# Kernel tuning notes

Measured on AMD Instinct MI355X. Metric: run time of the kernel, lower is better.

## Reference

```python
import jax, jax.numpy as jnp
import numpy as np

B, T, C, HS = 8, 2048, 768, 256  # batch, seq(block_size), n_embed, head_size


def setup_inputs() -> dict:
    key = jax.random.key(0)
    kx, kq, kk, kv = jax.random.split(key, 4)
    scale = 1.0 / np.sqrt(C)
    return {
        "x": jax.random.normal(kx, (B, T, C), dtype=jnp.float32),
        # torch nn.Linear(n_embed, head_size, bias=False) computes x @ W.T;
        # store weights pre-transposed as [in, out].
        "Wq": jax.random.normal(kq, (C, HS), dtype=jnp.float32) * scale,
        "Wk": jax.random.normal(kk, (C, HS), dtype=jnp.float32) * scale,
        "Wv": jax.random.normal(kv, (C, HS), dtype=jnp.float32) * scale,
    }


def reference(x, Wq, Wk, Wv):
    Bx, Tx, Cx = x.shape
    q = x @ Wq  # [B,T,HS]
    k = x @ Wk  # [B,T,HS]
    v = x @ Wv  # [B,T,HS]
    # NOTE: original scales by C**-0.5 with C = n_embed (not head_size)
    att = jnp.einsum('btd,bsd->bts', q, k) * (Cx ** -0.5)  # [B,T,T]
    causal = jnp.tril(jnp.ones((Tx, Tx), dtype=bool))
    att = jnp.where(causal, att, -jnp.inf)
    probs = jax.nn.softmax(att, axis=-1)
    # dropout=0.0 -> identity (eval mode)
    out = jnp.einsum('bts,bsd->btd', probs, v)  # [B,T,HS]
    return out
```

## Files before the change

kernel.cpp:

```cpp
#include <hip/hip_runtime.h>
#include <hip/hip_bf16.h>
#include <math.h>

#define B_  8
#define T_  2048
#define C_  768
#define HS_ 256

#define CHUNKS_PER_BATCH 72
#define NSLOT (CHUNKS_PER_BATCH * B_)

typedef float  f32x4  __attribute__((ext_vector_type(4)));
typedef __bf16 bf16x8 __attribute__((ext_vector_type(8)));
typedef __bf16 bf16x4 __attribute__((ext_vector_type(4)));
typedef __bf16 bf16x2 __attribute__((ext_vector_type(2)));

#define MFMA16(a, b, c) __builtin_amdgcn_mfma_f32_16x16x32_bf16((a), (b), (c), 0, 0, 0)

#define GLOAD_LDS16(gp, lp)                                                     \
    __builtin_amdgcn_global_load_lds(                                           \
        (const __attribute__((address_space(1))) void*)(gp),                    \
        (__attribute__((address_space(3))) void*)(lp), 16, 0, 0)

__device__ __forceinline__ int chunk_cum128(int qb) {
    int g = qb >> 1;
    return g * (g + 1) + (qb & 1) * (g + 1);
}

__global__ __launch_bounds__(256) void prep_kernel(const float* __restrict__ x,
                                                   const float* __restrict__ Wq,
                                                   const float* __restrict__ Wk,
                                                   const float* __restrict__ Wv,
                                                   __bf16* __restrict__ xb,
                                                   __bf16* __restrict__ wt_all,
                                                   float qscale) {
    const int bid = blockIdx.x;
    if (bid < 6144) {
        size_t i = ((size_t)bid * 256 + threadIdx.x) * 8;
        f32x4 a = *(const f32x4*)(x + i);
        f32x4 b = *(const f32x4*)(x + i + 4);
        bf16x8 o;
        o[0] = (__bf16)a[0]; o[1] = (__bf16)a[1]; o[2] = (__bf16)a[2]; o[3] = (__bf16)a[3];
        o[4] = (__bf16)b[0]; o[5] = (__bf16)b[1]; o[6] = (__bf16)b[2]; o[7] = (__bf16)b[3];
        *(bf16x8*)(xb + i) = o;
    } else {
        int idx = (bid - 6144) * 256 + threadIdx.x;
        int n   = idx & 255;
        int t   = idx >> 8;
        int mat = t / 96;
        int k8  = t - mat * 96;
        const float* W = (mat == 0) ? Wq : ((mat == 1) ? Wk : Wv);
        float scale = (mat == 0) ? qscale : 1.0f;
        bf16x8 o;
#pragma unroll
        for (int j = 0; j < 8; j++)
            o[j] = (__bf16)(W[(k8 * 8 + j) * HS_ + n] * scale);
        *(bf16x8*)&wt_all[((size_t)mat * HS_ + n) * C_ + k8 * 8] = o;
    }
}

__global__ __launch_bounds__(256) void proj_kernel(const __bf16* __restrict__ xb,
                                                   const __bf16* __restrict__ wt,
                                                   __bf16* __restrict__ qf_,
                                                   __bf16* __restrict__ kf_,
                                                   __bf16* __restrict__ vf_) {
    __shared__ alignas(16) __bf16 ldsA[2][128 * 32];
    __shared__ alignas(16) __bf16 ldsB[2][128 * 32];

    const int tid  = threadIdx.x;
    const int w    = tid >> 6;
    const int lane = tid & 63;
    const int cm   = lane & 15;
    const int quad = lane >> 4;
    const int wm   = w & 1;
    const int wn   = w >> 1;
    const int m0   = blockIdx.x * 128;
    const int n0   = blockIdx.y * 128;
    const int mat  = n0 >> 8;

    f32x4 acc[4][4];
#pragma unroll
    for (int i = 0; i < 4; i++)
#pragma unroll
        for (int j = 0; j < 4; j++) acc[i][j] = (f32x4){0.f, 0.f, 0.f, 0.f};

#pragma unroll
    for (int h = 0; h < 2; h++) {
        int c = tid + h * 256;
        GLOAD_LDS16(xb + (size_t)(m0 + (c >> 2)) * C_ + (c & 3) * 8, &ldsA[0][c * 8]);
        GLOAD_LDS16(wt + (size_t)(n0 + (c >> 2)) * C_ + (c & 3) * 8, &ldsB[0][c * 8]);
    }

    for (int kt = 0; kt < 24; kt++) {
        const int cur = kt & 1;
        __syncthreads();

        if (kt < 23) {
            const int k0 = (kt + 1) * 32;
#pragma unroll
            for (int h = 0; h < 2; h++) {
                int c = tid + h * 256;
                GLOAD_LDS16(xb + (size_t)(m0 + (c >> 2)) * C_ + k0 + (c & 3) * 8,
                            &ldsA[cur ^ 1][c * 8]);
                GLOAD_LDS16(wt + (size_t)(n0 + (c >> 2)) * C_ + k0 + (c & 3) * 8,
                            &ldsB[cur ^ 1][c * 8]);
            }
        }

        bf16x8 af[4], bfr[4];
#pragma unroll
        for (int mt = 0; mt < 4; mt++)
            af[mt] = *(const bf16x8*)&ldsA[cur][(wm * 64 + mt * 16 + cm) * 32 + quad * 8];
#pragma unroll
        for (int nt = 0; nt < 4; nt++)
            bfr[nt] = *(const bf16x8*)&ldsB[cur][(wn * 64 + nt * 16 + cm) * 32 + quad * 8];
        if (mat < 2) {
#pragma unroll
            for (int dt = 0; dt < 4; dt++)
#pragma unroll
                for (int qt2 = 0; qt2 < 4; qt2++)
                    acc[dt][qt2] = MFMA16(bfr[dt], af[qt2], acc[dt][qt2]);
        } else {
#pragma unroll
            for (int mt = 0; mt < 4; mt++)
#pragma unroll
                for (int nt = 0; nt < 4; nt++)
                    acc[mt][nt] = MFMA16(af[mt], bfr[nt], acc[mt][nt]);
        }
    }

    const int dBase = (n0 & 255) + wn * 64;
    const int b     = m0 >> 11;
    if (mat < 2) {
        const int rt2 = ((m0 & 2047) >> 6) + wm;
        __bf16* dst = (mat == 0) ? qf_ : kf_;
#pragma unroll
        for (int dt = 0; dt < 4; dt++)
#pragma unroll
            for (int qt2 = 0; qt2 < 4; qt2++) {
                int d0    = dBase + dt * 16 + quad * 4;
                int ksq   = d0 >> 5;
                int quadp = (d0 >> 3) & 3;
                int j0    = d0 & 7;
                size_t addr;
                if (mat == 0)
                    addr = ((((size_t)(b * 32 + rt2) * 4 + qt2) * 8 + ksq) * 64
                            + quadp * 16 + cm) * 8 + j0;
                else
                    addr = ((((size_t)(b * 32 + rt2) * 8 + ksq) * 4 + qt2) * 64
                            + quadp * 16 + cm) * 8 + j0;
                bf16x4 v4;
                v4[0] = (__bf16)acc[dt][qt2][0]; v4[1] = (__bf16)acc[dt][qt2][1];
                v4[2] = (__bf16)acc[dt][qt2][2]; v4[3] = (__bf16)acc[dt][qt2][3];
                *(bf16x4*)(dst + addr) = v4;
            }
    } else {
        const int rt = ((m0 & 2047) + wm * 64) >> 6;
#pragma unroll
        for (int mt = 0; mt < 4; mt++) {
            int ks2   = (mt >> 1) & 1;
            int quadF = (mt & 1) * 2 + (quad >> 1);
            int jb    = (quad & 1) * 4;
#pragma unroll
            for (int nt = 0; nt < 4; nt++) {
                int ntv = (dBase >> 4) + nt;
                size_t idx = ((((size_t)(b * 32 + rt) * 2 + ks2) * 16 + ntv) * 64
                              + quadF * 16 + cm) * 8 + jb;
                bf16x4 v4;
                v4[0] = (__bf16)acc[mt][nt][0]; v4[1] = (__bf16)acc[mt][nt][1];
                v4[2] = (__bf16)acc[mt][nt][2]; v4[3] = (__bf16)acc[mt][nt][3];
                *(bf16x4*)(vf_ + idx) = v4;
            }
        }
    }
}

__global__ __launch_bounds__(256, 2) void flash_part(const __bf16* __restrict__ qf_,
                                                     const __bf16* __restrict__ kf_,
                                                     const __bf16* __restrict__ vf_,
                                                     __bf16* __restrict__ Opart,
                                                     float* __restrict__ mpart,
                                                     float* __restrict__ lpart) {
    __shared__ alignas(16) __bf16 ldsK[2][8 * 2 * 64 * 8];
    __shared__ alignas(16) __bf16 ldsV[2][16 * 64 * 8];
    __shared__ alignas(16) __bf16 ldsP[4][2][512];

    const int tid  = threadIdx.x;
    const int w    = tid >> 6;
    const int lane = tid & 63;
    const int cm   = lane & 15;
    const int quad = lane >> 4;

    const int pid  = blockIdx.x;
    const int b    = pid & 7;
    const int r    = (CHUNKS_PER_BATCH - 1) - (pid >> 3);
    int qb = 0, ci = 0;
    {
        int rr = r;
        for (int j = 0; j < 16; j++) {
            int c = (j >> 1) + 1;
            if (rr < c) { qb = j; ci = rr; break; }
            rr -= c;
        }
    }
    const int lpid = b * CHUNKS_PER_BATCH + r;
    const int kt_begin = ci * 8;
    const int kt_end   = min(kt_begin + 8, 4 * qb + 4);

    bf16x8 qf2[2][8];
#pragma unroll
    for (int qg = 0; qg < 2; qg++) {
        int g16 = qb * 8 + w * 2 + qg;
        const __bf16* qp = qf_ + (((size_t)(b * 32 + (g16 >> 2)) * 4 + (g16 & 3)) * 8) * 512
                           + lane * 8;
#pragma unroll
        for (int ks = 0; ks < 8; ks++) qf2[qg][ks] = *(const bf16x8*)(qp + ks * 512);
    }

    auto stage = [&](int bsel, int kt) {
        const int kt64 = kt >> 1, kh = kt & 1;
        const __bf16* kgb = kf_ + (((size_t)(b * 32 + kt64) * 8) * 4 + kh * 2) * 512;
#pragma unroll
        for (int h = 0; h < 4; h++) {
            int g = h * 256 + tid;
            int ks = g >> 7, sub = g & 127;
            GLOAD_LDS16(kgb + (size_t)ks * 4 * 512 + sub * 8,
                        &ldsK[bsel][(h * 256 + w * 64) * 8]);
        }
        const __bf16* vgb = vf_ + ((size_t)(b * 64 + kt) * 16) * 512;
#pragma unroll
        for (int h = 0; h < 4; h++) {
            int g = h * 256 + tid;
            GLOAD_LDS16(vgb + (size_t)g * 8,
                        &ldsV[bsel][(h * 256 + w * 64) * 8]);
        }
    };

    f32x4 accO[2][16];
#pragma unroll
    for (int qg = 0; qg < 2; qg++)
#pragma unroll
        for (int i = 0; i < 16; i++) accO[qg][i] = (f32x4){0.f, 0.f, 0.f, 0.f};
    float mi[2] = {0.f, 0.f}, li[2] = {0.f, 0.f};

    const int wrow = qb * 128 + w * 32;

    stage(0, kt_begin);
    asm volatile("s_waitcnt vmcnt(0)" ::: "memory");
    __builtin_amdgcn_s_barrier();

    int cur = 0;
    for (int kt = kt_begin; kt < kt_end; kt++) {
        if (kt + 1 < kt_end) stage(cur ^ 1, kt + 1);

        f32x4 s[2][2];
#pragma unroll
        for (int ns = 0; ns < 2; ns++)
#pragma unroll
            for (int qg = 0; qg < 2; qg++) s[ns][qg] = (f32x4){0.f, 0.f, 0.f, 0.f};
        __builtin_amdgcn_s_setprio(1);
#pragma unroll
        for (int ns = 0; ns < 2; ns++)
#pragma unroll
            for (int ks = 0; ks < 8; ks++) {
                bf16x8 kfr = *(const bf16x8*)&ldsK[cur][(ks * 2 + ns) * 512 + lane * 8];
                s[ns][0] = MFMA16(kfr, qf2[0][ks], s[ns][0]);
                s[ns][1] = MFMA16(kfr, qf2[1][ks], s[ns][1]);
            }
        __builtin_amdgcn_s_setprio(0);
        if (kt * 32 + 31 > wrow) {
#pragma unroll
            for (int qg = 0; qg < 2; qg++) {
                int qglob = wrow + qg * 16 + cm;
#pragma unroll
                for (int ns = 0; ns < 2; ns++)
#pragma unroll
                    for (int i = 0; i < 4; i++)
                        if (kt * 32 + ns * 16 + quad * 4 + i > qglob)
                            s[ns][qg][i] = -__builtin_inff();
            }
        }
        if (kt == kt_begin) {
#pragma unroll
            for (int qg = 0; qg < 2; qg++) {
                float pm = -__builtin_inff();
#pragma unroll
                for (int ns = 0; ns < 2; ns++)
#pragma unroll
                    for (int i = 0; i < 4; i++) pm = fmaxf(pm, s[ns][qg][i]);
                pm = fmaxf(pm, __shfl_xor(pm, 16));
                pm = fmaxf(pm, __shfl_xor(pm, 32));
                mi[qg] = pm;
            }
        }
        float p[2][2][4];
        float rs[2] = {0.f, 0.f};
#pragma unroll
        for (int qg = 0; qg < 2; qg++)
#pragma unroll
            for (int ns = 0; ns < 2; ns++)
#pragma unroll
                for (int i = 0; i < 4; i++) {
                    p[qg][ns][i] = exp2f(s[ns][qg][i] - mi[qg]);
                    rs[qg] += p[qg][ns][i];
                }
#pragma unroll
        for (int qg = 0; qg < 2; qg++) {
            rs[qg] += __shfl_xor(rs[qg], 16);
            rs[qg] += __shfl_xor(rs[qg], 32);
            li[qg] += rs[qg];
        }

#pragma unroll
        for (int qg = 0; qg < 2; qg++)
#pragma unroll
            for (int ns = 0; ns < 2; ns++)
#pragma unroll
                for (int i2 = 0; i2 < 2; i2++) {
                    bf16x2 d2;
                    d2[0] = (__bf16)p[qg][ns][2 * i2];
                    d2[1] = (__bf16)p[qg][ns][2 * i2 + 1];
                    int off = ((ns * 2 + (quad >> 1)) * 16 + cm) * 8
                              + (quad & 1) * 4 + i2 * 2;
                    *(bf16x2*)&ldsP[w][qg][off] = d2;
                }
        bf16x8 pf0 = *(const bf16x8*)&ldsP[w][0][(quad * 16 + cm) * 8];
        bf16x8 pf1 = *(const bf16x8*)&ldsP[w][1][(quad * 16 + cm) * 8];
        __builtin_amdgcn_s_setprio(1);
#pragma unroll
        for (int nt = 0; nt < 16; nt++) {
            bf16x8 vfr = *(const bf16x8*)&ldsV[cur][(nt * 64 + lane) * 8];
            accO[0][nt] = MFMA16(vfr, pf0, accO[0][nt]);
            accO[1][nt] = MFMA16(vfr, pf1, accO[1][nt]);
        }
        __builtin_amdgcn_s_setprio(0);

        asm volatile("s_waitcnt vmcnt(0)" ::: "memory");
        __builtin_amdgcn_s_barrier();
        cur ^= 1;
    }

#pragma unroll
    for (int qg = 0; qg < 2; qg++) {
        __bf16* op = Opart + ((size_t)lpid * 128 + w * 32 + qg * 16 + cm) * HS_;
#pragma unroll
        for (int nt = 0; nt < 16; nt++) {
            bf16x4 v4;
            v4[0] = (__bf16)accO[qg][nt][0]; v4[1] = (__bf16)accO[qg][nt][1];
            v4[2] = (__bf16)accO[qg][nt][2]; v4[3] = (__bf16)accO[qg][nt][3];
            *(bf16x4*)(op + nt * 16 + quad * 4) = v4;
        }
        if (quad == 0) {
            mpart[lpid * 128 + w * 32 + qg * 16 + cm] = mi[qg];
            lpart[lpid * 128 + w * 32 + qg * 16 + cm] = li[qg];
        }
    }
}

__global__ __launch_bounds__(256) void flash_combine(const __bf16* __restrict__ Opart,
                                                     const float* __restrict__ mpart,
                                                     const float* __restrict__ lpart,
                                                     float* __restrict__ out) {
    const int b    = blockIdx.x >> 4;
    const int qb   = blockIdx.x & 15;
    const int nc   = (qb >> 1) + 1;
    const int pid0 = b * CHUNKS_PER_BATCH + chunk_cum128(qb);

    const int tid  = threadIdx.x;
    const int col  = (tid & 63) * 4;
    const int r0   = blockIdx.y * 16 + (tid >> 6) * 4;

    f32x4 ms = (f32x4){-__builtin_inff(), -__builtin_inff(),
                       -__builtin_inff(), -__builtin_inff()};
    for (int c = 0; c < nc; c++) {
        f32x4 m4 = *(const f32x4*)(mpart + (pid0 + c) * 128 + r0);
#pragma unroll
        for (int i = 0; i < 4; i++) ms[i] = fmaxf(ms[i], m4[i]);
    }
    f32x4 acc[4];
#pragma unroll
    for (int i = 0; i < 4; i++) acc[i] = (f32x4){0.f, 0.f, 0.f, 0.f};
    f32x4 lt = (f32x4){0.f, 0.f, 0.f, 0.f};
    for (int c = 0; c < nc; c++) {
        f32x4 m4 = *(const f32x4*)(mpart + (pid0 + c) * 128 + r0);
        f32x4 l4 = *(const f32x4*)(lpart + (pid0 + c) * 128 + r0);
#pragma unroll
        for (int i = 0; i < 4; i++) {
            float sc = exp2f(m4[i] - ms[i]);
            lt[i] += l4[i] * sc;
            bf16x4 o = *(const bf16x4*)(Opart
                        + ((size_t)(pid0 + c) * 128 + r0 + i) * HS_ + col);
            acc[i][0] += (float)o[0] * sc; acc[i][1] += (float)o[1] * sc;
            acc[i][2] += (float)o[2] * sc; acc[i][3] += (float)o[3] * sc;
        }
    }
#pragma unroll
    for (int i = 0; i < 4; i++) {
        float inv = 1.0f / lt[i];
        f32x4 res = (f32x4){acc[i][0] * inv, acc[i][1] * inv,
                            acc[i][2] * inv, acc[i][3] * inv};
        *(f32x4*)(out + ((size_t)(b * T_ + qb * 128 + r0 + i)) * HS_ + col) = res;
    }
}

extern "C" void kernel_launch(void* const* d_in, const int* in_sizes, int n_in,
                              void* d_out, int out_size, void* d_ws, size_t ws_size,
                              hipStream_t stream) {
    const float* x  = (const float*)d_in[0];
    const float* Wq = (const float*)d_in[1];
    const float* Wk = (const float*)d_in[2];
    const float* Wv = (const float*)d_in[3];
    float* out = (float*)d_out;

    char* ws = (char*)d_ws;
    size_t off = 0;
    __bf16* wt_all = (__bf16*)(ws + off); off += 1179648;
    __bf16* qfrag  = (__bf16*)(ws + off); off += 8388608;
    __bf16* kfrag  = (__bf16*)(ws + off); off += 8388608;
    __bf16* vfrag  = (__bf16*)(ws + off); off += 8388608;
    __bf16* xb     = (__bf16*)(ws + off);
    __bf16* Opart  = (__bf16*)(ws + off); off += (size_t)NSLOT * 128 * HS_ * 2;
    float*  mpart  = (float*)(ws + off);  off += (size_t)NSLOT * 128 * 4;
    float*  lpart  = (float*)(ws + off);

    float qscale = 1.4426950408889634f / sqrtf((float)C_);

    prep_kernel<<<dim3(6432), 256, 0, stream>>>(x, Wq, Wk, Wv, xb, wt_all, qscale);
    proj_kernel<<<dim3(128, 6), 256, 0, stream>>>(xb, wt_all, qfrag, kfrag, vfrag);
    flash_part<<<dim3(NSLOT), 256, 0, stream>>>(qfrag, kfrag, vfrag, Opart, mpart, lpart);
    flash_combine<<<dim3(128, 8), 256, 0, stream>>>(Opart, mpart, lpart, out);
}
```

Measured before the change: 187.6 us.

## Decouple waves in flash_part with per-wave 32-row chunks and private LDS

Each wave now owns its own 32-query-row work item with its own key range and its own LDS slot, instead of four waves sharing a 128-row block with a double-buffered K/V tile and block-wide barriers. K and V are loaded into a single per-wave buffer one after the other, so each wave waits on its own loads but never on a barrier. This removes barrier stalls and the extra work of waves whose rows are already past the causal diagonal. In exchange, K/V tiles are no longer shared across the four waves, so global/L2 traffic rises, and load latency is only partly hidden. The combine kernel is rewritten to merge the finer 32-row partials.

```diff
diff --git a/kernel.cpp b/kernel.cpp
--- a/kernel.cpp
+++ b/kernel.cpp
@@ -7,8 +7,8 @@
 #define C_  768
 #define HS_ 256
 
-#define CHUNKS_PER_BATCH 72
-#define NSLOT (CHUNKS_PER_BATCH * B_)
+#define WAVES_PER_BATCH 288
+#define NSLOT (WAVES_PER_BATCH * B_)
 
 typedef float  f32x4  __attribute__((ext_vector_type(4)));
 typedef __bf16 bf16x8 __attribute__((ext_vector_type(8)));
@@ -21,11 +21,6 @@
     __builtin_amdgcn_global_load_lds(                                           \
         (const __attribute__((address_space(1))) void*)(gp),                    \
         (__attribute__((address_space(3))) void*)(lp), 16, 0, 0)
-
-__device__ __forceinline__ int chunk_cum128(int qb) {
-    int g = qb >> 1;
-    return g * (g + 1) + (qb & 1) * (g + 1);
-}
 
 __global__ __launch_bounds__(256) void prep_kernel(const float* __restrict__ x,
                                                    const float* __restrict__ Wq,
@@ -181,8 +176,7 @@
                                                      __bf16* __restrict__ Opart,
                                                      float* __restrict__ mpart,
                                                      float* __restrict__ lpart) {
-    __shared__ alignas(16) __bf16 ldsK[2][8 * 2 * 64 * 8];
-    __shared__ alignas(16) __bf16 ldsV[2][16 * 64 * 8];
+    __shared__ alignas(16) __bf16 ldsKV[4][8192];
     __shared__ alignas(16) __bf16 ldsP[4][2][512];
 
     const int tid  = threadIdx.x;
@@ -191,49 +185,47 @@
     const int cm   = lane & 15;
     const int quad = lane >> 4;
 
-    const int pid  = blockIdx.x;
-    const int b    = pid & 7;
-    const int r    = (CHUNKS_PER_BATCH - 1) - (pid >> 3);
-    int qb = 0, ci = 0;
+    const int pid = blockIdx.x;
+    const int b   = pid & 7;
+    const int r   = (WAVES_PER_BATCH - 1) - ((pid >> 3) * 4 + w);
+    int g32 = 0, ci = 0;
     {
         int rr = r;
-        for (int j = 0; j < 16; j++) {
-            int c = (j >> 1) + 1;
-            if (rr < c) { qb = j; ci = rr; break; }
+        for (int j = 0; j < 64; j++) {
+            int c = (j >> 3) + 1;
+            if (rr < c) { g32 = j; ci = rr; break; }
             rr -= c;
         }
     }
-    const int lpid = b * CHUNKS_PER_BATCH + r;
+    const int lpid     = b * WAVES_PER_BATCH + r;
     const int kt_begin = ci * 8;
-    const int kt_end   = min(kt_begin + 8, 4 * qb + 4);
+    const int kt_end   = min(kt_begin + 8, g32 + 1);
+
+    __bf16* myKV = &ldsKV[w][0];
 
     bf16x8 qf2[2][8];
 #pragma unroll
     for (int qg = 0; qg < 2; qg++) {
-        int g16 = qb * 8 + w * 2 + qg;
+        int g16 = g32 * 2 + qg;
         const __bf16* qp = qf_ + (((size_t)(b * 32 + (g16 >> 2)) * 4 + (g16 & 3)) * 8) * 512
                            + lane * 8;
 #pragma unroll
         for (int ks = 0; ks < 8; ks++) qf2[qg][ks] = *(const bf16x8*)(qp + ks * 512);
     }
 
-    auto stage = [&](int bsel, int kt) {
+    auto stageK = [&](int kt) {
         const int kt64 = kt >> 1, kh = kt & 1;
         const __bf16* kgb = kf_ + (((size_t)(b * 32 + kt64) * 8) * 4 + kh * 2) * 512;
 #pragma unroll
-        for (int h = 0; h < 4; h++) {
-            int g = h * 256 + tid;
-            int ks = g >> 7, sub = g & 127;
-            GLOAD_LDS16(kgb + (size_t)ks * 4 * 512 + sub * 8,
-                        &ldsK[bsel][(h * 256 + w * 64) * 8]);
-        }
+        for (int u = 0; u < 16; u++)
+            GLOAD_LDS16(kgb + (size_t)(u >> 1) * 2048 + (u & 1) * 512 + lane * 8,
+                        myKV + u * 512);
+    };
+    auto stageV = [&](int kt) {
         const __bf16* vgb = vf_ + ((size_t)(b * 64 + kt) * 16) * 512;
 #pragma unroll
-        for (int h = 0; h < 4; h++) {
-            int g = h * 256 + tid;
-            GLOAD_LDS16(vgb + (size_t)g * 8,
-                        &ldsV[bsel][(h * 256 + w * 64) * 8]);
-        }
+        for (int u = 0; u < 16; u++)
+            GLOAD_LDS16(vgb + (size_t)u * 512 + lane * 8, myKV + u * 512);
     };
 
     f32x4 accO[2][16];
@@ -243,15 +235,11 @@
         for (int i = 0; i < 16; i++) accO[qg][i] = (f32x4){0.f, 0.f, 0.f, 0.f};
     float mi[2] = {0.f, 0.f}, li[2] = {0.f, 0.f};
 
-    const int wrow = qb * 128 + w * 32;
-
-    stage(0, kt_begin);
-    asm volatile("s_waitcnt vmcnt(0)" ::: "memory");
-    __builtin_amdgcn_s_barrier();
-
-    int cur = 0;
+    const int wrow = g32 * 32;
+
+    stageK(kt_begin);
     for (int kt = kt_begin; kt < kt_end; kt++) {
-        if (kt + 1 < kt_end) stage(cur ^ 1, kt + 1);
+        asm volatile("s_waitcnt vmcnt(0)" ::: "memory");
 
         f32x4 s[2][2];
 #pragma unroll
@@ -263,11 +251,14 @@
         for (int ns = 0; ns < 2; ns++)
 #pragma unroll
             for (int ks = 0; ks < 8; ks++) {
-                bf16x8 kfr = *(const bf16x8*)&ldsK[cur][(ks * 2 + ns) * 512 + lane * 8];
+                bf16x8 kfr = *(const bf16x8*)&myKV[(ks * 2 + ns) * 512 + lane * 8];
                 s[ns][0] = MFMA16(kfr, qf2[0][ks], s[ns][0]);
                 s[ns][1] = MFMA16(kfr, qf2[1][ks], s[ns][1]);
             }
         __builtin_amdgcn_s_setprio(0);
+        asm volatile("s_waitcnt lgkmcnt(0)" ::: "memory");
+        stageV(kt);
+
         if (kt * 32 + 31 > wrow) {
 #pragma unroll
             for (int qg = 0; qg < 2; qg++) {
@@ -326,23 +317,23 @@
                 }
         bf16x8 pf0 = *(const bf16x8*)&ldsP[w][0][(quad * 16 + cm) * 8];
         bf16x8 pf1 = *(const bf16x8*)&ldsP[w][1][(quad * 16 + cm) * 8];
+
+        asm volatile("s_waitcnt vmcnt(0)" ::: "memory");
         __builtin_amdgcn_s_setprio(1);
 #pragma unroll
         for (int nt = 0; nt < 16; nt++) {
-            bf16x8 vfr = *(const bf16x8*)&ldsV[cur][(nt * 64 + lane) * 8];
+            bf16x8 vfr = *(const bf16x8*)&myKV[nt * 512 + lane * 8];
             accO[0][nt] = MFMA16(vfr, pf0, accO[0][nt]);
             accO[1][nt] = MFMA16(vfr, pf1, accO[1][nt]);
         }
         __builtin_amdgcn_s_setprio(0);
-
-        asm volatile("s_waitcnt vmcnt(0)" ::: "memory");
-        __builtin_amdgcn_s_barrier();
-        cur ^= 1;
+        asm volatile("s_waitcnt lgkmcnt(0)" ::: "memory");
+        if (kt + 1 < kt_end) stageK(kt + 1);
     }
 
 #pragma unroll
     for (int qg = 0; qg < 2; qg++) {
-        __bf16* op = Opart + ((size_t)lpid * 128 + w * 32 + qg * 16 + cm) * HS_;
+        __bf16* op = Opart + ((size_t)lpid * 32 + qg * 16 + cm) * HS_;
 #pragma unroll
         for (int nt = 0; nt < 16; nt++) {
             bf16x4 v4;
@@ -351,8 +342,8 @@
             *(bf16x4*)(op + nt * 16 + quad * 4) = v4;
         }
         if (quad == 0) {
-            mpart[lpid * 128 + w * 32 + qg * 16 + cm] = mi[qg];
-            lpart[lpid * 128 + w * 32 + qg * 16 + cm] = li[qg];
+            mpart[lpid * 32 + qg * 16 + cm] = mi[qg];
+            lpart[lpid * 32 + qg * 16 + cm] = li[qg];
         }
     }
 }
@@ -361,45 +352,46 @@
                                                      const float* __restrict__ mpart,
                                                      const float* __restrict__ lpart,
                                                      float* __restrict__ out) {
-    const int b    = blockIdx.x >> 4;
-    const int qb   = blockIdx.x & 15;
-    const int nc   = (qb >> 1) + 1;
-    const int pid0 = b * CHUNKS_PER_BATCH + chunk_cum128(qb);
-
-    const int tid  = threadIdx.x;
-    const int col  = (tid & 63) * 4;
-    const int r0   = blockIdx.y * 16 + (tid >> 6) * 4;
-
-    f32x4 ms = (f32x4){-__builtin_inff(), -__builtin_inff(),
-                       -__builtin_inff(), -__builtin_inff()};
+    const int b    = blockIdx.x >> 6;
+    const int g    = blockIdx.x & 63;
+    const int t    = g >> 3;
+    const int nc   = t + 1;
+    const int pid0 = b * WAVES_PER_BATCH + 4 * t * (t + 1) + (g & 7) * (t + 1);
+
+    const int tid = threadIdx.x;
+    const int col = (tid & 63) * 4;
+    const int r0  = (tid >> 6) * 8;
+
+    float ms[8];
+#pragma unroll
+    for (int i = 0; i < 8; i++) ms[i] = -__builtin_inff();
+    for (int c = 0; c < nc; c++)
+#pragma unroll
+        for (int i = 0; i < 8; i++)
+            ms[i] = fmaxf(ms[i], mpart[(pid0 + c) * 32 + r0 + i]);
+
+    f32x4 acc[8];
+    float lt[8];
+#pragma unroll
+    for (int i = 0; i < 8; i++) { acc[i] = (f32x4){0.f, 0.f, 0.f, 0.f}; lt[i] = 0.f; }
+
     for (int c = 0; c < nc; c++) {
-        f32x4 m4 = *(const f32x4*)(mpart + (pid0 + c) * 128 + r0);
-#pragma unroll
-        for (int i = 0; i < 4; i++) ms[i] = fmaxf(ms[i], m4[i]);
-    }
-    f32x4 acc[4];
-#pragma unroll
-    for (int i = 0; i < 4; i++) acc[i] = (f32x4){0.f, 0.f, 0.f, 0.f};
-    f32x4 lt = (f32x4){0.f, 0.f, 0.f, 0.f};
-    for (int c = 0; c < nc; c++) {
-        f32x4 m4 = *(const f32x4*)(mpart + (pid0 + c) * 128 + r0);
-        f32x4 l4 = *(const f32x4*)(lpart + (pid0 + c) * 128 + r0);
-#pragma unroll
-        for (int i = 0; i < 4; i++) {
-            float sc = exp2f(m4[i] - ms[i]);
-            lt[i] += l4[i] * sc;
+#pragma unroll
+        for (int i = 0; i < 8; i++) {
+            float sc = exp2f(mpart[(pid0 + c) * 32 + r0 + i] - ms[i]);
+            lt[i] += lpart[(pid0 + c) * 32 + r0 + i] * sc;
             bf16x4 o = *(const bf16x4*)(Opart
-                        + ((size_t)(pid0 + c) * 128 + r0 + i) * HS_ + col);
+                        + ((size_t)(pid0 + c) * 32 + r0 + i) * HS_ + col);
             acc[i][0] += (float)o[0] * sc; acc[i][1] += (float)o[1] * sc;
             acc[i][2] += (float)o[2] * sc; acc[i][3] += (float)o[3] * sc;
         }
     }
 #pragma unroll
-    for (int i = 0; i < 4; i++) {
+    for (int i = 0; i < 8; i++) {
         float inv = 1.0f / lt[i];
         f32x4 res = (f32x4){acc[i][0] * inv, acc[i][1] * inv,
                             acc[i][2] * inv, acc[i][3] * inv};
-        *(f32x4*)(out + ((size_t)(b * T_ + qb * 128 + r0 + i)) * HS_ + col) = res;
+        *(f32x4*)(out + ((size_t)(b * T_ + g * 32 + r0 + i)) * HS_ + col) = res;
     }
 }
 
@@ -419,14 +411,14 @@
     __bf16* kfrag  = (__bf16*)(ws + off); off += 8388608;
     __bf16* vfrag  = (__bf16*)(ws + off); off += 8388608;
     __bf16* xb     = (__bf16*)(ws + off);
-    __bf16* Opart  = (__bf16*)(ws + off); off += (size_t)NSLOT * 128 * HS_ * 2;
-    float*  mpart  = (float*)(ws + off);  off += (size_t)NSLOT * 128 * 4;
+    __bf16* Opart  = (__bf16*)(ws + off); off += (size_t)NSLOT * 32 * HS_ * 2;
+    float*  mpart  = (float*)(ws + off);  off += (size_t)NSLOT * 32 * 4;
     float*  lpart  = (float*)(ws + off);
 
     float qscale = 1.4426950408889634f / sqrtf((float)C_);
 
     prep_kernel<<<dim3(6432), 256, 0, stream>>>(x, Wq, Wk, Wv, xb, wt_all, qscale);
     proj_kernel<<<dim3(128, 6), 256, 0, stream>>>(xb, wt_all, qfrag, kfrag, vfrag);
-    flash_part<<<dim3(NSLOT), 256, 0, stream>>>(qfrag, kfrag, vfrag, Opart, mpart, lpart);
-    flash_combine<<<dim3(128, 8), 256, 0, stream>>>(Opart, mpart, lpart, out);
+    flash_part<<<dim3(576), 256, 0, stream>>>(qfrag, kfrag, vfrag, Opart, mpart, lpart);
+    flash_combine<<<dim3(512), 256, 0, stream>>>(Opart, mpart, lpart, out);
 }
```

New measurement: 202.1 us. 7.7% more time.
